# Optimization experiments

Hardware: AMD Instinct MI355X
Metric: run time of the kernel (lower is better)

The kernel has to match this reference:

```python
import jax, jax.numpy as jnp
import numpy as np

B, L, D, A, OUT, HID_FC = 4, 4096, 128, 16, 2, 24


def setup_inputs() -> dict:
    key = jax.random.key(0)
    ks = jax.random.split(key, 8)
    xn = lambda k, shape: (jax.random.normal(k, shape, dtype=jnp.float32)
                           * np.sqrt(2.0 / (shape[0] + shape[1])))
    return {
        "x": jax.random.normal(ks[0], (B, L, D), dtype=jnp.float32),
        "fc1_w": xn(ks[1], (D, D)),
        "fc1_b": jnp.zeros((D,), dtype=jnp.float32),
        "Wq_w": xn(ks[2], (D, D)),
        "Wk_w": xn(ks[3], (D, D)),
        "Wv_w": xn(ks[4], (D, D)),
        "fc2_w": xn(ks[5], (D, HID_FC)),
        "fc2_b": jnp.zeros((HID_FC,), dtype=jnp.float32),
        "fc3_w": xn(ks[6], (HID_FC, OUT)),
        "fc3_b": jnp.zeros((OUT,), dtype=jnp.float32),
        "atten_size": A,
        "hidden_size": D,
    }


def _attention(x, Wq_w, Wk_w, Wv_w, atten_size, sqrt_hidden):
    b, l, d = x.shape
    W = 2 * atten_size + 1
    # zero-pad sequence dim, then gather local windows.
    # Faithful to roll-based construction: x_nei[b,i,j] = x[b, i + atten_size - j] (0 if out of range)
    padded = jnp.pad(x, ((0, 0), (atten_size, atten_size), (0, 0)))
    idx = jnp.arange(l)[:, None] + 2 * atten_size - jnp.arange(W)[None, :]  # [L, W]
    x_nei = padded[:, idx]                      # [B, L, W, D]
    q = (x @ Wq_w)[:, :, None, :]               # [B, L, 1, D]
    k = x_nei @ Wk_w                            # [B, L, W, D]
    dsc = jnp.einsum('blod,blwd->blow', q, k) / sqrt_hidden  # [B, L, 1, W]
    # Original torch code: Softmax(dim=2) over the singleton dim -> all-ones (faithful)
    a = jax.nn.softmax(dsc, axis=2)             # [B, L, 1, W]
    v = x_nei @ Wv_w                            # [B, L, W, D]
    out = jnp.squeeze(a @ v, axis=2)            # [B, L, D]
    return out, a


def reference(x, fc1_w, fc1_b, Wq_w, Wk_w, Wv_w, fc2_w, fc2_b, fc3_w, fc3_b,
              atten_size, hidden_size):
    sqrt_hidden = np.sqrt(float(hidden_size))
    h = jax.nn.relu(x @ fc1_w + fc1_b)
    h, a = _attention(h, Wq_w, Wk_w, Wv_w, atten_size, sqrt_hidden)
    h = jax.nn.relu(h @ fc2_w + fc2_b)
    out = h @ fc3_w + fc3_b
    return out, a
```

## Files before the change

kernel.cpp:

```cpp
#include <hip/hip_runtime.h>

constexpr int Bv   = 4;
constexpr int Lv   = 4096;
constexpr int Dv   = 128;
constexpr int Av   = 16;
constexpr int Wwin = 2*Av + 1;
constexpr int OUTv = 2;
constexpr int HIDv = 24;
constexpr int NROWS = Bv * Lv;

constexpr int TILE  = 32;
constexpr int SROWS = TILE + 2*Av;
constexpr int NBLK  = NROWS / TILE;

typedef __attribute__((ext_vector_type(8))) short short8;
typedef __attribute__((ext_vector_type(4))) short short4v;
typedef __attribute__((ext_vector_type(4))) float f32x4;

__device__ __forceinline__ short f2bf(float f) {
    unsigned u = __builtin_bit_cast(unsigned, f);
    u += 0x7FFFu + ((u >> 16) & 1u);
    return (short)(u >> 16);
}

__global__ __launch_bounds__(256) void k_prep(const float* __restrict__ W1,
                                              const float* __restrict__ Wv,
                                              const float* __restrict__ fc2,
                                              short* __restrict__ W1T,
                                              short* __restrict__ WfT) {
    const int b = blockIdx.x, t = threadIdx.x;
    if (b < 16) {
        __shared__ float st[32][36];
        const int bi = b >> 2, bj = b & 3;
        const int r = t >> 3, q = t & 7;
        const float4 v = *(const float4*)&W1[(size_t)(bi*32 + r)*Dv + bj*32 + q*4];
        st[r][q*4+0] = v.x; st[r][q*4+1] = v.y; st[r][q*4+2] = v.z; st[r][q*4+3] = v.w;
        __syncthreads();
        short4v o;
        o[0] = f2bf(st[q*4+0][r]);
        o[1] = f2bf(st[q*4+1][r]);
        o[2] = f2bf(st[q*4+2][r]);
        o[3] = f2bf(st[q*4+3][r]);
        *(short4v*)&W1T[(size_t)(bj*32 + r)*Dv + bi*32 + q*4] = o;
    } else {
        const int i = (b - 16)*256 + t;
        const int n = i & 31, k = i >> 5;
        float acc = 0.f;
        if (n < HIDv) {
#pragma unroll 8
            for (int j = 0; j < Dv; ++j)
                acc = fmaf(Wv[(size_t)k*Dv + j], fc2[(size_t)j*HIDv + n], acc);
        }
        WfT[(size_t)n*Dv + k] = f2bf(acc);
    }
}

__global__ __launch_bounds__(256) void k_fused(const float* __restrict__ x,
                                               const float* __restrict__ b1,
                                               const float* __restrict__ fc2b,
                                               const float* __restrict__ fc3w,
                                               const float* __restrict__ fc3b,
                                               const short* __restrict__ W1T,
                                               const short* __restrict__ WfT,
                                               float* __restrict__ out,
                                               float* __restrict__ aout) {
    __shared__ short sA[SROWS][136];
    __shared__ float smv[SROWS][25];
    __shared__ float sh2[TILE][25];
    __shared__ float sb1[Dv];

    const int t = threadIdx.x, blk = blockIdx.x;
    const int g0 = blk * TILE;
    const int bb = g0 >> 12;
    const int l0 = g0 & (Lv - 1);
    const int lane = t & 63, w = t >> 6;

    for (int i = t; i < SROWS*32; i += 256) {
        const int r = i >> 5, c4 = i & 31;
        const int l = l0 - Av + r;
        short4v o = {0, 0, 0, 0};
        if (l >= 0 && l < Lv) {
            const float4 v = *(const float4*)&x[((size_t)bb*Lv + l)*Dv + c4*4];
            o[0] = f2bf(v.x); o[1] = f2bf(v.y); o[2] = f2bf(v.z); o[3] = f2bf(v.w);
        }
        *(short4v*)&sA[r][c4*4] = o;
    }
    if (t < Dv) sb1[t] = b1[t];

    {
        float4* a4 = (float4*)aout;
        const float4 one4 = {1.f, 1.f, 1.f, 1.f};
        for (int i = t; i < 264; i += 256)
            a4[(size_t)blk*264 + i] = one4;
    }
    __syncthreads();

    const int ncol0 = w * 32;
    const int arow  = lane & 15;
    const int kgrp  = (lane >> 4) * 8;

    f32x4 acc[4][2];
#pragma unroll
    for (int mf = 0; mf < 4; ++mf) { acc[mf][0] = (f32x4){0,0,0,0}; acc[mf][1] = (f32x4){0,0,0,0}; }

#pragma unroll
    for (int kb = 0; kb < 4; ++kb) {
        const int kof = kb*32 + kgrp;
        const short8 bf0 = *(const short8*)&W1T[(size_t)(ncol0 +      arow)*Dv + kof];
        const short8 bf1 = *(const short8*)&W1T[(size_t)(ncol0 + 16 + arow)*Dv + kof];
#pragma unroll
        for (int mf = 0; mf < 4; ++mf) {
            const short8 af = *(const short8*)&sA[mf*16 + arow][kof];
            acc[mf][0] = __builtin_amdgcn_mfma_f32_16x16x32_bf16(af, bf0, acc[mf][0], 0, 0, 0);
            acc[mf][1] = __builtin_amdgcn_mfma_f32_16x16x32_bf16(af, bf1, acc[mf][1], 0, 0, 0);
        }
    }
    __syncthreads();

    const int crow = (lane >> 4) * 4;
#pragma unroll
    for (int mf = 0; mf < 4; ++mf) {
#pragma unroll
        for (int nf = 0; nf < 2; ++nf) {
            const int col  = ncol0 + nf*16 + arow;
            const float bias = sb1[col];
#pragma unroll
            for (int r = 0; r < 4; ++r) {
                float h = acc[mf][nf][r] + bias;
                h = h > 0.f ? h : 0.f;
                sA[mf*16 + crow + r][col] = f2bf(h);
            }
        }
    }
    __syncthreads();

    f32x4 acc2[2];
    acc2[0] = (f32x4){0,0,0,0};
    acc2[1] = (f32x4){0,0,0,0};
#pragma unroll
    for (int pp = 0; pp < 2; ++pp) {
        const int p = w*2 + pp, mf = p >> 1, nf = p & 1;
#pragma unroll
        for (int kb = 0; kb < 4; ++kb) {
            const int kof = kb*32 + kgrp;
            const short8 af = *(const short8*)&sA[mf*16 + arow][kof];
            const short8 bf = *(const short8*)&WfT[(size_t)(nf*16 + arow)*Dv + kof];
            acc2[pp] = __builtin_amdgcn_mfma_f32_16x16x32_bf16(af, bf, acc2[pp], 0, 0, 0);
        }
    }
#pragma unroll
    for (int pp = 0; pp < 2; ++pp) {
        const int p = w*2 + pp, mf = p >> 1, nf = p & 1;
        const int col = nf*16 + arow;
        if (col < HIDv) {
#pragma unroll
            for (int r = 0; r < 4; ++r) {
                const int row = mf*16 + crow + r;
                const int l = l0 - Av + row;
                smv[row][col] = (l >= 0 && l < Lv) ? acc2[pp][r] : 0.f;
            }
        }
    }
    __syncthreads();

    if (t < 96) {
        const int c = t % 24, rg = t / 24;
        const int rb = rg * 8;
        float s = 0.f;
#pragma unroll
        for (int ww = 0; ww < Wwin; ++ww) s += smv[rb + ww][c];
        const float bias = fc2b[c];
#pragma unroll
        for (int r2 = 0; r2 < 8; ++r2) {
            const int rr = rb + r2;
            const float h = s + bias;
            sh2[rr][c] = h > 0.f ? h : 0.f;
            if (r2 < 7) s += smv[rr + Wwin][c] - smv[rr][c];
        }
    }
    __syncthreads();

    if (t < TILE*OUTv) {
        const int r = t >> 1, oc = t & 1;
        float a = fc3b[oc];
#pragma unroll
        for (int c = 0; c < HIDv; ++c)
            a = fmaf(sh2[r][c], fc3w[c*OUTv + oc], a);
        out[(size_t)(g0 + r)*OUTv + oc] = a;
    }
}

extern "C" void kernel_launch(void* const* d_in, const int* in_sizes, int n_in,
                              void* d_out, int out_size, void* d_ws, size_t ws_size,
                              hipStream_t stream) {
    const float* x     = (const float*)d_in[0];
    const float* fc1_w = (const float*)d_in[1];
    const float* fc1_b = (const float*)d_in[2];
    const float* Wv_w  = (const float*)d_in[5];
    const float* fc2_w = (const float*)d_in[6];
    const float* fc2_b = (const float*)d_in[7];
    const float* fc3_w = (const float*)d_in[8];
    const float* fc3_b = (const float*)d_in[9];

    float* out  = (float*)d_out;
    float* aout = (float*)d_out + NROWS * OUTv;

    short* W1T = (short*)d_ws;
    short* WfT = (short*)d_ws + 16384;

    k_prep<<<dim3(32), dim3(256), 0, stream>>>(fc1_w, Wv_w, fc2_w, W1T, WfT);
    k_fused<<<dim3(NBLK), dim3(256), 0, stream>>>(x, fc1_b, fc2_b, fc3_w, fc3_b,
                                                  W1T, WfT, out, aout);
}
```

Measured before the change: 18.10 us.

## Fuse weight prep into main kernel, computing Wv·fc2 per block via MFMA

```diff
diff --git a/kernel.cpp b/kernel.cpp
--- a/kernel.cpp
+++ b/kernel.cpp
@@ -23,48 +23,18 @@
     return (short)(u >> 16);
 }
 
-__global__ __launch_bounds__(256) void k_prep(const float* __restrict__ W1,
-                                              const float* __restrict__ Wv,
-                                              const float* __restrict__ fc2,
-                                              short* __restrict__ W1T,
-                                              short* __restrict__ WfT) {
-    const int b = blockIdx.x, t = threadIdx.x;
-    if (b < 16) {
-        __shared__ float st[32][36];
-        const int bi = b >> 2, bj = b & 3;
-        const int r = t >> 3, q = t & 7;
-        const float4 v = *(const float4*)&W1[(size_t)(bi*32 + r)*Dv + bj*32 + q*4];
-        st[r][q*4+0] = v.x; st[r][q*4+1] = v.y; st[r][q*4+2] = v.z; st[r][q*4+3] = v.w;
-        __syncthreads();
-        short4v o;
-        o[0] = f2bf(st[q*4+0][r]);
-        o[1] = f2bf(st[q*4+1][r]);
-        o[2] = f2bf(st[q*4+2][r]);
-        o[3] = f2bf(st[q*4+3][r]);
-        *(short4v*)&W1T[(size_t)(bj*32 + r)*Dv + bi*32 + q*4] = o;
-    } else {
-        const int i = (b - 16)*256 + t;
-        const int n = i & 31, k = i >> 5;
-        float acc = 0.f;
-        if (n < HIDv) {
-#pragma unroll 8
-            for (int j = 0; j < Dv; ++j)
-                acc = fmaf(Wv[(size_t)k*Dv + j], fc2[(size_t)j*HIDv + n], acc);
-        }
-        WfT[(size_t)n*Dv + k] = f2bf(acc);
-    }
-}
-
-__global__ __launch_bounds__(256) void k_fused(const float* __restrict__ x,
-                                               const float* __restrict__ b1,
-                                               const float* __restrict__ fc2b,
-                                               const float* __restrict__ fc3w,
-                                               const float* __restrict__ fc3b,
-                                               const short* __restrict__ W1T,
-                                               const short* __restrict__ WfT,
-                                               float* __restrict__ out,
-                                               float* __restrict__ aout) {
+__global__ __launch_bounds__(256) void k_all(const float* __restrict__ x,
+                                             const float* __restrict__ W1,
+                                             const float* __restrict__ b1,
+                                             const float* __restrict__ Wv,
+                                             const float* __restrict__ fc2,
+                                             const float* __restrict__ fc2b,
+                                             const float* __restrict__ fc3w,
+                                             const float* __restrict__ fc3b,
+                                             float* __restrict__ out,
+                                             float* __restrict__ aout) {
     __shared__ short sA[SROWS][136];
+    __shared__ short sWfT[32][136];
     __shared__ float smv[SROWS][25];
     __shared__ float sh2[TILE][25];
     __shared__ float sb1[Dv];
@@ -74,6 +44,9 @@
     const int bb = g0 >> 12;
     const int l0 = g0 & (Lv - 1);
     const int lane = t & 63, w = t >> 6;
+    const int arow = lane & 15;
+    const int kgrp = (lane >> 4) * 8;
+    const int crow = (lane >> 4) * 4;
 
     for (int i = t; i < SROWS*32; i += 256) {
         const int r = i >> 5, c4 = i & 31;
@@ -93,12 +66,54 @@
         for (int i = t; i < 264; i += 256)
             a4[(size_t)blk*264 + i] = one4;
     }
+
+    {
+        f32x4 accW[2][2];
+#pragma unroll
+        for (int a = 0; a < 2; ++a) { accW[a][0] = (f32x4){0,0,0,0}; accW[a][1] = (f32x4){0,0,0,0}; }
+#pragma unroll
+        for (int kb = 0; kb < 4; ++kb) {
+            const int kof = kb*32 + kgrp;
+            short8 bW[2];
+#pragma unroll
+            for (int nf = 0; nf < 2; ++nf) {
+                const int n = nf*16 + arow;
+#pragma unroll
+                for (int j = 0; j < 8; ++j) {
+                    const float v = (n < HIDv) ? fc2[(size_t)(kof + j)*HIDv + n] : 0.f;
+                    bW[nf][j] = f2bf(v);
+                }
+            }
+#pragma unroll
+            for (int mf2 = 0; mf2 < 2; ++mf2) {
+                const int m = (w*2 + mf2)*16 + arow;
+                const float4 v0 = *(const float4*)&Wv[(size_t)m*Dv + kof];
+                const float4 v1 = *(const float4*)&Wv[(size_t)m*Dv + kof + 4];
+                short8 aW;
+                aW[0] = f2bf(v0.x); aW[1] = f2bf(v0.y); aW[2] = f2bf(v0.z); aW[3] = f2bf(v0.w);
+                aW[4] = f2bf(v1.x); aW[5] = f2bf(v1.y); aW[6] = f2bf(v1.z); aW[7] = f2bf(v1.w);
+                accW[mf2][0] = __builtin_amdgcn_mfma_f32_16x16x32_bf16(aW, bW[0], accW[mf2][0], 0, 0, 0);
+                accW[mf2][1] = __builtin_amdgcn_mfma_f32_16x16x32_bf16(aW, bW[1], accW[mf2][1], 0, 0, 0);
+            }
+        }
+#pragma unroll
+        for (int mf2 = 0; mf2 < 2; ++mf2) {
+#pragma unroll
+            for (int nf = 0; nf < 2; ++nf) {
+                const int n = nf*16 + arow;
+                const int m = (w*2 + mf2)*16 + crow;
+                short4v o;
+                o[0] = f2bf(accW[mf2][nf][0]);
+                o[1] = f2bf(accW[mf2][nf][1]);
+                o[2] = f2bf(accW[mf2][nf][2]);
+                o[3] = f2bf(accW[mf2][nf][3]);
+                *(short4v*)&sWfT[n][m] = o;
+            }
+        }
+    }
     __syncthreads();
 
     const int ncol0 = w * 32;
-    const int arow  = lane & 15;
-    const int kgrp  = (lane >> 4) * 8;
-
     f32x4 acc[4][2];
 #pragma unroll
     for (int mf = 0; mf < 4; ++mf) { acc[mf][0] = (f32x4){0,0,0,0}; acc[mf][1] = (f32x4){0,0,0,0}; }
@@ -106,8 +121,15 @@
 #pragma unroll
     for (int kb = 0; kb < 4; ++kb) {
         const int kof = kb*32 + kgrp;
-        const short8 bf0 = *(const short8*)&W1T[(size_t)(ncol0 +      arow)*Dv + kof];
-        const short8 bf1 = *(const short8*)&W1T[(size_t)(ncol0 + 16 + arow)*Dv + kof];
+        short8 bf0, bf1;
+        {
+            const int n0 = ncol0 + arow, n1 = ncol0 + 16 + arow;
+#pragma unroll
+            for (int j = 0; j < 8; ++j) {
+                bf0[j] = f2bf(W1[(size_t)(kof + j)*Dv + n0]);
+                bf1[j] = f2bf(W1[(size_t)(kof + j)*Dv + n1]);
+            }
+        }
 #pragma unroll
         for (int mf = 0; mf < 4; ++mf) {
             const short8 af = *(const short8*)&sA[mf*16 + arow][kof];
@@ -117,7 +139,6 @@
     }
     __syncthreads();
 
-    const int crow = (lane >> 4) * 4;
 #pragma unroll
     for (int mf = 0; mf < 4; ++mf) {
 #pragma unroll
@@ -144,7 +165,7 @@
         for (int kb = 0; kb < 4; ++kb) {
             const int kof = kb*32 + kgrp;
             const short8 af = *(const short8*)&sA[mf*16 + arow][kof];
-            const short8 bf = *(const short8*)&WfT[(size_t)(nf*16 + arow)*Dv + kof];
+            const short8 bf = *(const short8*)&sWfT[nf*16 + arow][kof];
             acc2[pp] = __builtin_amdgcn_mfma_f32_16x16x32_bf16(af, bf, acc2[pp], 0, 0, 0);
         }
     }
@@ -205,10 +226,6 @@
     float* out  = (float*)d_out;
     float* aout = (float*)d_out + NROWS * OUTv;
 
-    short* W1T = (short*)d_ws;
-    short* WfT = (short*)d_ws + 16384;
-
-    k_prep<<<dim3(32), dim3(256), 0, stream>>>(fc1_w, Wv_w, fc2_w, W1T, WfT);
-    k_fused<<<dim3(NBLK), dim3(256), 0, stream>>>(x, fc1_b, fc2_b, fc3_w, fc3_b,
-                                                  W1T, WfT, out, aout);
+    k_all<<<dim3(NBLK), dim3(256), 0, stream>>>(x, fc1_w, fc1_b, Wv_w, fc2_w,
+                                                fc2_b, fc3_w, fc3_b, out, aout);
 }
```

Measured after the change: 16.39 us. 1.1x faster.
